# Kernel optimization log

Measured on AMD Instinct MI355X. Metric: run time of the kernel, lower is better.

The kernel has to match this reference:

```python
import jax, jax.numpy as jnp
import numpy as np

N_EMBD = 768
D_STATE = 64
D_CONV = 4
EXPAND = 2
D_INNER = N_EMBD * EXPAND  # 1536
DT_RANK = max(D_STATE // 16, 1)  # 4
BATCH, SEQ = 16, 512


def setup_inputs() -> dict:
    key = jax.random.key(0)
    ks = jax.random.split(key, 10)
    s = lambda fan_in: 1.0 / np.sqrt(fan_in)
    x = jax.random.normal(ks[0], (BATCH, SEQ, N_EMBD), dtype=jnp.float32)
    W_in = jax.random.uniform(ks[1], (N_EMBD, 2 * D_INNER), minval=-s(N_EMBD), maxval=s(N_EMBD))
    conv_w = jax.random.uniform(ks[2], (D_INNER, D_CONV), minval=-s(D_CONV), maxval=s(D_CONV))
    conv_b = jax.random.uniform(ks[3], (D_INNER,), minval=-s(D_CONV), maxval=s(D_CONV))
    W_x = jax.random.uniform(ks[4], (D_INNER, DT_RANK + 2 * D_STATE), minval=-s(D_INNER), maxval=s(D_INNER))
    W_dt = jax.random.uniform(ks[5], (DT_RANK, D_INNER), minval=-s(DT_RANK), maxval=s(DT_RANK))
    b_dt = jax.random.uniform(ks[6], (D_INNER,), minval=-s(DT_RANK), maxval=s(DT_RANK))
    # A_log = log(arange(1, N+1)) repeated per channel (S4D-real init)
    A_log = jnp.tile(jnp.log(jnp.arange(1, D_STATE + 1, dtype=jnp.float32))[None, :], (D_INNER, 1))
    Dp = jnp.ones((D_INNER,), dtype=jnp.float32)
    W_out = jax.random.uniform(ks[7], (D_INNER, N_EMBD), minval=-s(D_INNER), maxval=s(D_INNER))
    return {"x": x, "W_in": W_in, "conv_w": conv_w, "conv_b": conv_b,
            "W_x": W_x, "W_dt": W_dt, "b_dt": b_dt, "A_log": A_log,
            "Dp": Dp, "W_out": W_out}


def _mamba_forward(x, W_in, conv_w, conv_b, W_x, W_dt, b_dt, A_log, Dp, W_out):
    Bsz, L, _ = x.shape
    d_inner = Dp.shape[0]
    n = A_log.shape[1]
    dt_rank = W_dt.shape[0]

    xr = x @ W_in                                  # (B, L, 2*d_inner)
    x_ssm, res = jnp.split(xr, 2, axis=-1)

    # causal depthwise conv1d
    xc = x_ssm.transpose(0, 2, 1)                  # (B, d_inner, L)
    kern = conv_w[:, None, :]                      # (d_inner, 1, K) grouped
    xc = jax.lax.conv_general_dilated(
        xc, kern, window_strides=(1,),
        padding=[(conv_w.shape[-1] - 1, 0)],
        feature_group_count=d_inner)
    xc = xc + conv_b[None, :, None]
    x_ssm = jax.nn.silu(xc.transpose(0, 2, 1))      # (B, L, d_inner)

    x_dbl = x_ssm @ W_x                            # (B, L, dt_rank + 2n)
    dlt = x_dbl[..., :dt_rank]
    Bv = x_dbl[..., dt_rank:dt_rank + n]           # (B, L, n)
    Cv = x_dbl[..., dt_rank + n:]                  # (B, L, n)
    delta = jax.nn.softplus(dlt @ W_dt + b_dt)     # (B, L, d_inner)

    A = -jnp.exp(A_log)                            # (d_inner, n)

    def step(h, inp):
        d_t, B_t, C_t, x_t = inp                   # (B,d_inner),(B,n),(B,n),(B,d_inner)
        dA = jnp.exp(d_t[:, :, None] * A)          # (B, d_inner, n)
        u = d_t[:, :, None] * B_t[:, None, :] * x_t[:, :, None]
        h = dA * h + u
        y_t = jnp.einsum('bn,bdn->bd', C_t, h)
        return h, y_t

    h0 = jnp.zeros((Bsz, d_inner, n), dtype=x.dtype)
    _, ys = jax.lax.scan(
        step, h0,
        (delta.transpose(1, 0, 2), Bv.transpose(1, 0, 2),
         Cv.transpose(1, 0, 2), x_ssm.transpose(1, 0, 2)))
    y = ys.transpose(1, 0, 2) + Dp * x_ssm         # (B, L, d_inner)

    out = (y * jax.nn.silu(res)) @ W_out           # (B, L, n_embd)
    return out


def reference(x, W_in, conv_w, conv_b, W_x, W_dt, b_dt, A_log, Dp, W_out):
    return _mamba_forward(x, W_in, conv_w, conv_b, W_x, W_dt, b_dt, A_log, Dp, W_out)
```

## Files before the change

### kernel.cpp

```cpp
#include <hip/hip_runtime.h>

using u16 = unsigned short;
typedef __bf16 bf16x8 __attribute__((ext_vector_type(8)));
typedef float f32x4 __attribute__((ext_vector_type(4)));
typedef float f32x2 __attribute__((ext_vector_type(2)));

__device__ __forceinline__ float bf2f(u16 u) {
  unsigned v = ((unsigned)u) << 16;
  float f;
  __builtin_memcpy(&f, &v, 4);
  return f;
}
__device__ __forceinline__ u16 f2bf(float f) {
  unsigned v;
  __builtin_memcpy(&v, &f, 4);
  v = v + 0x7FFFu + ((v >> 16) & 1u);
  return (u16)(v >> 16);
}

#define GLL16(gp, lp)                                            \
  __builtin_amdgcn_global_load_lds(                              \
      (const __attribute__((address_space(1))) void*)(gp),       \
      (__attribute__((address_space(3))) void*)(lp), 16, 0, 0)

#define DPP_ADD(v, ctrl)                                                      \
  ((v) + __int_as_float(__builtin_amdgcn_update_dpp(                          \
             0, __float_as_int(v), (ctrl), 0xf, 0xf, true)))

__device__ __forceinline__ f32x2 pk_fma(f32x2 a, f32x2 b, f32x2 c) {
  return __builtin_elementwise_fma(a, b, c);
}
#define VLO(v) __builtin_shufflevector((v), (v), 0, 1)
#define VHI(v) __builtin_shufflevector((v), (v), 2, 3)

__global__ __launch_bounds__(256) void split_bf16_kernel(
    const float* __restrict__ X, u16* __restrict__ H, u16* __restrict__ L) {
  const int i4 = (blockIdx.x * 256 + threadIdx.x) << 2;
  const float4 v = *(const float4*)(X + i4);
  ushort4 h, l;
  h.x = f2bf(v.x); l.x = f2bf(v.x - bf2f(h.x));
  h.y = f2bf(v.y); l.y = f2bf(v.y - bf2f(h.y));
  h.z = f2bf(v.z); l.z = f2bf(v.z - bf2f(h.z));
  h.w = f2bf(v.w); l.w = f2bf(v.w - bf2f(h.w));
  *(ushort4*)(H + i4) = h;
  *(ushort4*)(L + i4) = l;
}

__global__ __launch_bounds__(256) void split_gate_kernel(
    const float* __restrict__ Y, const float* __restrict__ sres,
    u16* __restrict__ H, u16* __restrict__ L) {
  const int i4 = (blockIdx.x * 256 + threadIdx.x) << 2;
  const float4 y = *(const float4*)(Y + i4);
  const float4 g = *(const float4*)(sres + i4);
  float4 v = make_float4(y.x * g.x, y.y * g.y, y.z * g.z, y.w * g.w);
  ushort4 h, l;
  h.x = f2bf(v.x); l.x = f2bf(v.x - bf2f(h.x));
  h.y = f2bf(v.y); l.y = f2bf(v.y - bf2f(h.y));
  h.z = f2bf(v.z); l.z = f2bf(v.z - bf2f(h.z));
  h.w = f2bf(v.w); l.w = f2bf(v.w - bf2f(h.w));
  *(ushort4*)(H + i4) = h;
  *(ushort4*)(L + i4) = l;
}

__global__ __launch_bounds__(256) void transpose_split_kernel(
    const float* __restrict__ W, int K, int N, u16* __restrict__ Thi,
    u16* __restrict__ Tlo) {
  __shared__ float t[32][33];
  const int tid = threadIdx.x;
  const int r = tid >> 3, c4 = (tid & 7) << 2;
  const float4 v = *(const float4*)(W + (size_t)(blockIdx.y * 32 + r) * N +
                                    blockIdx.x * 32 + c4);
  t[r][c4 + 0] = v.x;
  t[r][c4 + 1] = v.y;
  t[r][c4 + 2] = v.z;
  t[r][c4 + 3] = v.w;
  __syncthreads();
  const float w0 = t[c4 + 0][r], w1 = t[c4 + 1][r];
  const float w2 = t[c4 + 2][r], w3 = t[c4 + 3][r];
  ushort4 h, l;
  h.x = f2bf(w0); l.x = f2bf(w0 - bf2f(h.x));
  h.y = f2bf(w1); l.y = f2bf(w1 - bf2f(h.y));
  h.z = f2bf(w2); l.z = f2bf(w2 - bf2f(h.z));
  h.w = f2bf(w3); l.w = f2bf(w3 - bf2f(h.w));
  const size_t o = (size_t)(blockIdx.x * 32 + r) * K + blockIdx.y * 32 + c4;
  *(ushort4*)(Thi + o) = h;
  *(ushort4*)(Tlo + o) = l;
}

template <int BM, int BN, int WM, int WN, int NTILES, int EPI>
__global__ __launch_bounds__(64 * WM * WN, 2) void gemm_pipe(
    const u16* __restrict__ Ahi, const u16* __restrict__ Alo,
    const u16* __restrict__ BThi, const u16* __restrict__ BTlo,
    float* __restrict__ C0, float* __restrict__ C1, int N, int nSplit) {
  constexpr int T = 64 * WM * WN;
  constexpr int K = NTILES * 32;
  constexpr int RW = BM / WM;
  constexpr int CW = BN / WN;
  constexpr int MT = RW / 16;
  constexpr int NC = CW / 16;
  constexpr int IA = BM / (T / 4);
  constexpr int IB = BN / (T / 4);
  constexpr int L = 2 * (IA + IB);
  constexpr int OAl = BM * 32;
  constexpr int OBh = 2 * BM * 32;
  constexpr int OBl = 2 * BM * 32 + BN * 32;
  constexpr int SBUF = 2 * (BM + BN) * 32;

  extern __shared__ u16 S[];

  const int tid = threadIdx.x;
  const int lane = tid & 63, wv = tid >> 6;
  const int wm = wv / WN, wn = wv % WN;
  const int bm0 = blockIdx.y * BM, bn0 = blockIdx.x * BN;
  const int fr = lane & 15, fq = lane >> 4;
  const int rq = tid >> 2;
  const int cq = (tid & 3) << 3;

  f32x4 acc[MT][NC];
#pragma unroll
  for (int i = 0; i < MT; ++i)
#pragma unroll
    for (int j = 0; j < NC; ++j) acc[i][j] = {0.f, 0.f, 0.f, 0.f};

  auto stage = [&](int kt, int sbuf) {
    const int k0 = kt * 32;
    u16* Sb = S + sbuf * SBUF;
#pragma unroll
    for (int i = 0; i < IA; ++i) {
      const size_t g = (size_t)(bm0 + i * (T / 4) + rq) * K + k0 + cq;
      const int lb = (i * (T / 4) + wv * 16) * 32;
      GLL16(Ahi + g, Sb + lb);
      GLL16(Alo + g, Sb + OAl + lb);
    }
#pragma unroll
    for (int i = 0; i < IB; ++i) {
      const size_t g = (size_t)(bn0 + i * (T / 4) + rq) * K + k0 + cq;
      const int lb = (i * (T / 4) + wv * 16) * 32;
      GLL16(BThi + g, Sb + OBh + lb);
      GLL16(BTlo + g, Sb + OBl + lb);
    }
  };

  stage(0, 0);
  stage(1, 1);
  asm volatile("s_waitcnt vmcnt(%0)" ::"i"(L) : "memory");
  __builtin_amdgcn_s_barrier();
  __builtin_amdgcn_sched_barrier(0);

  int cb = 0, sb = 2;
#pragma unroll 3
  for (int t = 0; t < NTILES; ++t) {
    if (t + 2 < NTILES) stage(t + 2, sb);

    const u16* Sb = S + cb * SBUF;
    bf16x8 fAh[MT], fAl[MT], fBh[NC], fBl[NC];
#pragma unroll
    for (int mt = 0; mt < MT; ++mt) {
      const int ao = (wm * RW + mt * 16 + fr) * 32 + fq * 8;
      fAh[mt] = *(const bf16x8*)&Sb[ao];
      fAl[mt] = *(const bf16x8*)&Sb[OAl + ao];
    }
#pragma unroll
    for (int nt = 0; nt < NC; ++nt) {
      const int bo = (wn * CW + nt * 16 + fr) * 32 + fq * 8;
      fBh[nt] = *(const bf16x8*)&Sb[OBh + bo];
      fBl[nt] = *(const bf16x8*)&Sb[OBl + bo];
    }

    __builtin_amdgcn_s_setprio(1);
#pragma unroll
    for (int mt = 0; mt < MT; ++mt)
#pragma unroll
      for (int nt = 0; nt < NC; ++nt) {
        acc[mt][nt] = __builtin_amdgcn_mfma_f32_16x16x32_bf16(
            fAh[mt], fBh[nt], acc[mt][nt], 0, 0, 0);
        acc[mt][nt] = __builtin_amdgcn_mfma_f32_16x16x32_bf16(
            fAh[mt], fBl[nt], acc[mt][nt], 0, 0, 0);
        acc[mt][nt] = __builtin_amdgcn_mfma_f32_16x16x32_bf16(
            fAl[mt], fBh[nt], acc[mt][nt], 0, 0, 0);
      }
    __builtin_amdgcn_s_setprio(0);

    if (t + 1 < NTILES) {
      if (t + 2 < NTILES) {
        asm volatile("s_waitcnt vmcnt(%0)" ::"i"(L) : "memory");
      } else {
        asm volatile("s_waitcnt vmcnt(0)" ::: "memory");
      }
      __builtin_amdgcn_s_barrier();
      __builtin_amdgcn_sched_barrier(0);
    }
    cb = cb == 2 ? 0 : cb + 1;
    sb = sb == 2 ? 0 : sb + 1;
  }

#pragma unroll
  for (int mt = 0; mt < MT; ++mt)
#pragma unroll
    for (int nt = 0; nt < NC; ++nt) {
      const int col = bn0 + wn * CW + nt * 16 + fr;
#pragma unroll
      for (int r = 0; r < 4; ++r) {
        const int row = bm0 + wm * RW + mt * 16 + fq * 4 + r;
        float v = acc[mt][nt][r];
        if (EPI == 1) {
          if (col < nSplit) {
            C0[(size_t)row * nSplit + col] = v;
          } else {
            v = v / (1.f + __expf(-v));
            C1[(size_t)row * (N - nSplit) + (col - nSplit)] = v;
          }
        } else {
          C0[(size_t)row * N + col] = v;
        }
      }
    }
}

__global__ __launch_bounds__(256) void conv_silu_kernel(
    const float* __restrict__ raw, const float* __restrict__ cw,
    const float* __restrict__ cb, float* __restrict__ xs) {
  const int i4 = (blockIdx.x * 256 + threadIdx.x) << 2;
  const int d = i4 % 1536;
  const int l = (i4 / 1536) & 511;
  const float4 wA = *(const float4*)(cw + (d << 2));
  const float4 wB = *(const float4*)(cw + (d << 2) + 4);
  const float4 wC = *(const float4*)(cw + (d << 2) + 8);
  const float4 wD = *(const float4*)(cw + (d << 2) + 12);
  float4 acc = *(const float4*)(cb + d);
  const float* p = raw + i4;
  const float4 x3 = *(const float4*)(p);
  acc.x = fmaf(x3.x, wA.w, acc.x);
  acc.y = fmaf(x3.y, wB.w, acc.y);
  acc.z = fmaf(x3.z, wC.w, acc.z);
  acc.w = fmaf(x3.w, wD.w, acc.w);
  if (l >= 3) {
    const float4 x0 = *(const float4*)(p - 4608);
    const float4 x1 = *(const float4*)(p - 3072);
    const float4 x2 = *(const float4*)(p - 1536);
    acc.x = fmaf(x0.x, wA.x, acc.x); acc.y = fmaf(x0.y, wB.x, acc.y);
    acc.z = fmaf(x0.z, wC.x, acc.z); acc.w = fmaf(x0.w, wD.x, acc.w);
    acc.x = fmaf(x1.x, wA.y, acc.x); acc.y = fmaf(x1.y, wB.y, acc.y);
    acc.z = fmaf(x1.z, wC.y, acc.z); acc.w = fmaf(x1.w, wD.y, acc.w);
    acc.x = fmaf(x2.x, wA.z, acc.x); acc.y = fmaf(x2.y, wB.z, acc.y);
    acc.z = fmaf(x2.z, wC.z, acc.z); acc.w = fmaf(x2.w, wD.z, acc.w);
  } else {
#pragma unroll
    for (int k = 0; k < 3; ++k) {
      if (l - 3 + k >= 0) {
        const float4 xk = *(const float4*)(p + (k - 3) * 1536);
        const float wkA = (&wA.x)[k], wkB = (&wB.x)[k];
        const float wkC = (&wC.x)[k], wkD = (&wD.x)[k];
        acc.x = fmaf(xk.x, wkA, acc.x);
        acc.y = fmaf(xk.y, wkB, acc.y);
        acc.z = fmaf(xk.z, wkC, acc.z);
        acc.w = fmaf(xk.w, wkD, acc.w);
      }
    }
  }
  float4 o;
  o.x = acc.x / (1.f + __expf(-acc.x));
  o.y = acc.y / (1.f + __expf(-acc.y));
  o.z = acc.z / (1.f + __expf(-acc.z));
  o.w = acc.w / (1.f + __expf(-acc.w));
  *(float4*)(xs + i4) = o;
}

__global__ __launch_bounds__(256) void gemm_x_kernel(
    const float* __restrict__ XS, const float* __restrict__ Wx,
    float* __restrict__ Xd) {
  __shared__ float rows[8 * 1536];
  const int tid = threadIdx.x;
  const float4* src = (const float4*)(XS + (size_t)blockIdx.x * (8 * 1536));
  float4* dst = (float4*)rows;
#pragma unroll
  for (int j = 0; j < 12; ++j) dst[tid + 256 * j] = src[tid + 256 * j];
  __syncthreads();
  if (tid < 132) {
    float acc[8];
#pragma unroll
    for (int r = 0; r < 8; ++r) acc[r] = 0.f;
    for (int k = 0; k < 1536; k += 4) {
      const float w0 = Wx[(k + 0) * 132 + tid];
      const float w1 = Wx[(k + 1) * 132 + tid];
      const float w2 = Wx[(k + 2) * 132 + tid];
      const float w3 = Wx[(k + 3) * 132 + tid];
#pragma unroll
      for (int r = 0; r < 8; ++r) {
        const float4 xr = *(const float4*)&rows[r * 1536 + k];
        acc[r] = fmaf(xr.x, w0, acc[r]);
        acc[r] = fmaf(xr.y, w1, acc[r]);
        acc[r] = fmaf(xr.z, w2, acc[r]);
        acc[r] = fmaf(xr.w, w3, acc[r]);
      }
    }
    float* out = Xd + (size_t)blockIdx.x * (8 * 132) + tid;
#pragma unroll
    for (int r = 0; r < 8; ++r) out[r * 132] = acc[r];
  }
}

__global__ __launch_bounds__(256) void delta_kernel(
    const float* __restrict__ Xd, const float* __restrict__ Wdt,
    const float* __restrict__ bdt, float* __restrict__ delta) {
  const int i4 = (blockIdx.x * 256 + threadIdx.x) << 2;
  const int d = i4 % 1536;
  const int bl = i4 / 1536;
  const float4 t = *(const float4*)(Xd + (size_t)bl * 132);
  const float4 W0 = *(const float4*)(Wdt + d);
  const float4 W1 = *(const float4*)(Wdt + 1536 + d);
  const float4 W2 = *(const float4*)(Wdt + 3072 + d);
  const float4 W3 = *(const float4*)(Wdt + 4608 + d);
  float4 z = *(const float4*)(bdt + d);
  z.x = fmaf(t.x, W0.x, z.x); z.y = fmaf(t.x, W0.y, z.y);
  z.z = fmaf(t.x, W0.z, z.z); z.w = fmaf(t.x, W0.w, z.w);
  z.x = fmaf(t.y, W1.x, z.x); z.y = fmaf(t.y, W1.y, z.y);
  z.z = fmaf(t.y, W1.z, z.z); z.w = fmaf(t.y, W1.w, z.w);
  z.x = fmaf(t.z, W2.x, z.x); z.y = fmaf(t.z, W2.y, z.y);
  z.z = fmaf(t.z, W2.z, z.z); z.w = fmaf(t.z, W2.w, z.w);
  z.x = fmaf(t.w, W3.x, z.x); z.y = fmaf(t.w, W3.y, z.y);
  z.z = fmaf(t.w, W3.z, z.z); z.w = fmaf(t.w, W3.w, z.w);
  float4 o;
  o.x = fmaxf(z.x, 0.f) + log1pf(__expf(-fabsf(z.x)));
  o.y = fmaxf(z.y, 0.f) + log1pf(__expf(-fabsf(z.y)));
  o.z = fmaxf(z.z, 0.f) + log1pf(__expf(-fabsf(z.z)));
  o.w = fmaxf(z.w, 0.f) + log1pf(__expf(-fabsf(z.w)));
  *(float4*)(delta + i4) = o;
}

__global__ __launch_bounds__(256) void scan_kernel(
    const float* __restrict__ delta, float* __restrict__ xs,
    const float* __restrict__ Xd, const float* __restrict__ Dp) {
  __shared__ float L[2][16 * 192];
  const int tid = threadIdx.x;
  const int lane = tid & 63;
  const int wv = tid >> 6;
  const int ln = (lane & 3) | ((lane >> 1) & 4);
  const int sub = ((lane >> 2) & 1) | ((lane >> 3) & 6);
  const int b = blockIdx.x / 48;
  const int dg = blockIdx.x - b * 48;
  const int dbase = dg << 5;
  const int ch = (wv << 3) + sub;
  const int d = dbase + ch;

  const float dp = Dp[d];
  const float cln = -(float)(8 * ln);

  const size_t blBase = (size_t)b * 512;
  float* pYl = xs + (blBase + (size_t)ln) * 1536 + d;

  int sj[4], sf[4];
#pragma unroll
  for (int s = 0; s < 4; ++s) {
    const int u = tid + (s << 8);
    sj[s] = u >> 6;
    sf[s] = u & 63;
  }

  const int idxD = 128 + ch;
  const int idxX = 160 + ch;
  const int ofsB = ln << 3;
  const int ofsC = 64 + (ln << 3);

  float4 st[4];
#define STAGE_LOAD(c)                                                         \
  {                                                                           \
    _Pragma("unroll") for (int s = 0; s < 4; ++s) {                           \
      const int f = sf[s];                                                    \
      if (f < 48) {                                                           \
        const size_t bl = blBase + ((c) << 4) + sj[s];                        \
        const float* src =                                                    \
            (f < 32) ? (Xd + bl * 132 + 4 + (f << 2))                         \
                     : ((f < 40) ? (delta + bl * 1536 + dbase + ((f - 32) << 2)) \
                                 : (xs + bl * 1536 + dbase + ((f - 40) << 2))); \
        st[s] = *(const float4*)src;                                          \
      }                                                                       \
    }                                                                         \
  }
#define STAGE_WRITE(c)                                                        \
  {                                                                           \
    float* Lb = &L[(c) & 1][0];                                               \
    _Pragma("unroll") for (int s = 0; s < 4; ++s) {                           \
      const int f = sf[s];                                                    \
      if (f < 48) {                                                           \
        const int di = sj[s] * 192 +                                          \
                       ((f < 32) ? (f << 2)                                   \
                                 : ((f < 40) ? (128 + ((f - 32) << 2))        \
                                             : (160 + ((f - 40) << 2))));     \
        *(float4*)&Lb[di] = st[s];                                            \
      }                                                                       \
    }                                                                         \
  }

  f32x2 H0 = {0.f, 0.f}, H1 = {0.f, 0.f}, H2 = {0.f, 0.f}, H3 = {0.f, 0.f};
  float yacc = 0.f;

  STAGE_LOAD(0);
  STAGE_WRITE(0);
  __syncthreads();

  for (int c = 0; c < 32; ++c) {
    if (c < 31) STAGE_LOAD(c + 1);
    const float* P = &L[c & 1][0];
#pragma unroll
    for (int j = 0; j < 16; ++j) {
      const float dl = P[j * 192 + idxD];
      const float xt = P[j * 192 + idxX];
      const f32x4 Bq0 = *(const f32x4*)&P[j * 192 + ofsB];
      const f32x4 Bq1 = *(const f32x4*)&P[j * 192 + ofsB + 4];
      const f32x4 Cq0 = *(const f32x4*)&P[j * 192 + ofsC];
      const f32x4 Cq1 = *(const f32x4*)&P[j * 192 + ofsC + 4];

      const float r = __expf(-dl);
      const float e0 = __expf(cln * dl);
      const float dx = dl * xt;
      const float r2 = r * r;
      f32x2 Q0;
      Q0[0] = e0 * r;
      Q0[1] = Q0[0] * r;
      const f32x2 r2v = {r2, r2};
      const f32x2 Q1 = Q0 * r2v;
      const f32x2 Q2 = Q1 * r2v;
      const f32x2 Q3 = Q2 * r2v;
      const f32x2 dxv = {dx, dx};

      H0 = pk_fma(Q0, H0, dxv * VLO(Bq0));
      H1 = pk_fma(Q1, H1, dxv * VHI(Bq0));
      H2 = pk_fma(Q2, H2, dxv * VLO(Bq1));
      H3 = pk_fma(Q3, H3, dxv * VHI(Bq1));

      f32x2 Pv = VLO(Cq0) * H0;
      Pv = pk_fma(VHI(Cq0), H1, Pv);
      Pv = pk_fma(VLO(Cq1), H2, Pv);
      Pv = pk_fma(VHI(Cq1), H3, Pv);
      float p = Pv[0] + Pv[1];
      p = DPP_ADD(p, 0xB1);
      p = DPP_ADD(p, 0x4E);
      p = DPP_ADD(p, 0x128);
      const float yv = fmaf(dp, xt, p);
      yacc = (ln == (j & 7)) ? yv : yacc;
      if ((j & 7) == 7) {
        pYl[(size_t)((c << 4) + (j & 8)) * 1536] = yacc;
      }
    }
    if (c < 31) STAGE_WRITE(c + 1);
    __syncthreads();
  }
#undef STAGE_LOAD
#undef STAGE_WRITE
}

extern "C" void kernel_launch(void* const* d_in, const int* in_sizes, int n_in,
                              void* d_out, int out_size, void* d_ws,
                              size_t ws_size, hipStream_t stream) {
  const float* x = (const float*)d_in[0];
  const float* W_in = (const float*)d_in[1];
  const float* conv_w = (const float*)d_in[2];
  const float* conv_b = (const float*)d_in[3];
  const float* W_x = (const float*)d_in[4];
  const float* W_dt = (const float*)d_in[5];
  const float* b_dt = (const float*)d_in[6];
  const float* Dp = (const float*)d_in[8];
  const float* W_out = (const float*)d_in[9];

  char* ws = (char*)d_ws;
  float* raw = (float*)(ws);
  char* Dreg = ws + 50331648;
  u16* xhi = (u16*)(Dreg);
  u16* xlo = (u16*)(Dreg + 12582912);
  u16* WinThi = (u16*)(Dreg + 25165824);
  u16* WinTlo = (u16*)(Dreg + 29884416);
  float* xs = (float*)(Dreg);
  float* res = (float*)(ws + 100663296);
  float* xdbl = (float*)(ws + 150994944);
  float* delta = raw;
  u16* yhi = (u16*)(ws);
  u16* ylo = (u16*)(ws + 25165824);
  u16* WoutThi = (u16*)(ws + 100663296);
  u16* WoutTlo = (u16*)(ws + 100663296 + 2359296);

  static bool attr_done = false;
  if (!attr_done) {
    hipFuncSetAttribute(
        reinterpret_cast<const void*>(&gemm_pipe<256, 128, 4, 2, 24, 1>),
        hipFuncAttributeMaxDynamicSharedMemorySize, 147456);
    hipFuncSetAttribute(
        reinterpret_cast<const void*>(&gemm_pipe<256, 128, 4, 2, 48, 0>),
        hipFuncAttributeMaxDynamicSharedMemorySize, 147456);
    attr_done = true;
  }

  dim3 blk(256);
  hipLaunchKernelGGL(split_bf16_kernel, dim3(6144), blk, 0, stream, x, xhi,
                     xlo);
  hipLaunchKernelGGL(transpose_split_kernel, dim3(96, 24), blk, 0, stream,
                     W_in, 768, 3072, WinThi, WinTlo);
  hipLaunchKernelGGL((gemm_pipe<256, 128, 4, 2, 24, 1>), dim3(24, 32),
                     dim3(512), 147456, stream, xhi, xlo, WinThi, WinTlo, raw,
                     res, 3072, 1536);
  hipLaunchKernelGGL(conv_silu_kernel, dim3(12288), blk, 0, stream, raw,
                     conv_w, conv_b, xs);
  hipLaunchKernelGGL(gemm_x_kernel, dim3(1024), blk, 0, stream, xs, W_x, xdbl);
  hipLaunchKernelGGL(delta_kernel, dim3(12288), blk, 0, stream, xdbl, W_dt,
                     b_dt, delta);
  hipLaunchKernelGGL(scan_kernel, dim3(768), blk, 0, stream, delta, xs, xdbl,
                     Dp);
  hipLaunchKernelGGL(split_gate_kernel, dim3(12288), blk, 0, stream, xs, res,
                     yhi, ylo);
  hipLaunchKernelGGL(transpose_split_kernel, dim3(24, 48), blk, 0, stream,
                     W_out, 1536, 768, WoutThi, WoutTlo);
  hipLaunchKernelGGL((gemm_pipe<256, 128, 4, 2, 48, 0>), dim3(6, 32),
                     dim3(512), 147456, stream, yhi, ylo, WoutThi, WoutTlo,
                     (float*)d_out, nullptr, 768, 0);
}
```

Baseline: 705.8 us.

## Move x_proj GEMM onto MFMA with split-bf16 three-pass emulation

Replaces the scalar fp32 x_ssm @ W_x kernel with an MFMA-based GEMM. It uses hi/lo bf16 splits of both operands and three products to keep close to fp32 accuracy. A new prep kernel transposes W_x into padded (144-row) hi/lo bf16 buffers in the workspace. The GEMM double-buffers LDS, converts A on the fly and stages B through global_load_lds. This adds an extra launch and a conversion step, and uses only 256 blocks of 128 threads.

```diff
diff --git a/kernel.cpp b/kernel.cpp
--- a/kernel.cpp
+++ b/kernel.cpp
@@ -87,6 +87,34 @@
   *(ushort4*)(Tlo + o) = l;
 }
 
+__global__ __launch_bounds__(256) void wxt_prep_kernel(
+    const float* __restrict__ Wx, u16* __restrict__ Thi,
+    u16* __restrict__ Tlo) {
+  __shared__ float t[32][33];
+  const int tid = threadIdx.x;
+  const int r = tid >> 3, c4 = (tid & 7) << 2;
+#pragma unroll
+  for (int j = 0; j < 4; ++j) {
+    const int n = blockIdx.x * 32 + c4 + j;
+    t[r][c4 + j] =
+        (n < 132) ? Wx[(size_t)(blockIdx.y * 32 + r) * 132 + n] : 0.f;
+  }
+  __syncthreads();
+  const int nrow = blockIdx.x * 32 + r;
+  if (nrow < 144) {
+    const float w0 = t[c4 + 0][r], w1 = t[c4 + 1][r];
+    const float w2 = t[c4 + 2][r], w3 = t[c4 + 3][r];
+    ushort4 h, l;
+    h.x = f2bf(w0); l.x = f2bf(w0 - bf2f(h.x));
+    h.y = f2bf(w1); l.y = f2bf(w1 - bf2f(h.y));
+    h.z = f2bf(w2); l.z = f2bf(w2 - bf2f(h.z));
+    h.w = f2bf(w3); l.w = f2bf(w3 - bf2f(h.w));
+    const size_t o = (size_t)nrow * 1536 + blockIdx.y * 32 + c4;
+    *(ushort4*)(Thi + o) = h;
+    *(ushort4*)(Tlo + o) = l;
+  }
+}
+
 template <int BM, int BN, int WM, int WN, int NTILES, int EPI>
 __global__ __launch_bounds__(64 * WM * WN, 2) void gemm_pipe(
     const u16* __restrict__ Ahi, const u16* __restrict__ Alo,
@@ -215,6 +243,111 @@
         }
       }
     }
+}
+
+__global__ __launch_bounds__(128) void gemm_xp_kernel(
+    const float* __restrict__ XS, const u16* __restrict__ BThi,
+    const u16* __restrict__ BTlo, float* __restrict__ Xd) {
+  __shared__ u16 sA[2][2][32 * 32];
+  __shared__ u16 sB[2][2][144 * 32];
+  const int tid = threadIdx.x;
+  const int lane = tid & 63, wv = tid >> 6;
+  const int bm0 = blockIdx.x << 5;
+  const int fr = lane & 15, fq = lane >> 4;
+  const int ar = tid >> 2, ac = (tid & 3) << 3;
+
+  f32x4 acc[9];
+#pragma unroll
+  for (int j = 0; j < 9; ++j) acc[j] = {0.f, 0.f, 0.f, 0.f};
+
+  const float* pA = XS + (size_t)(bm0 + ar) * 1536 + ac;
+
+  float4 xa0, xa1;
+  auto loadA = [&](int k0) {
+    xa0 = *(const float4*)(pA + k0);
+    xa1 = *(const float4*)(pA + k0 + 4);
+  };
+  auto writeA = [&](int buf) {
+    ushort4 h0, h1, l0, l1;
+    h0.x = f2bf(xa0.x); l0.x = f2bf(xa0.x - bf2f(h0.x));
+    h0.y = f2bf(xa0.y); l0.y = f2bf(xa0.y - bf2f(h0.y));
+    h0.z = f2bf(xa0.z); l0.z = f2bf(xa0.z - bf2f(h0.z));
+    h0.w = f2bf(xa0.w); l0.w = f2bf(xa0.w - bf2f(h0.w));
+    h1.x = f2bf(xa1.x); l1.x = f2bf(xa1.x - bf2f(h1.x));
+    h1.y = f2bf(xa1.y); l1.y = f2bf(xa1.y - bf2f(h1.y));
+    h1.z = f2bf(xa1.z); l1.z = f2bf(xa1.z - bf2f(h1.z));
+    h1.w = f2bf(xa1.w); l1.w = f2bf(xa1.w - bf2f(h1.w));
+    u16* Ah = &sA[buf][0][ar * 32 + ac];
+    u16* Al = &sA[buf][1][ar * 32 + ac];
+    *(ushort4*)Ah = h0;
+    *(ushort4*)(Ah + 4) = h1;
+    *(ushort4*)Al = l0;
+    *(ushort4*)(Al + 4) = l1;
+  };
+  auto stageB = [&](int k0, int buf) {
+#pragma unroll
+    for (int i = 0; i < 5; ++i) {
+      const int ch = i * 128 + tid;
+      if (ch < 576) {
+        const int row = ch >> 2, cq = (ch & 3) << 3;
+        const size_t g = (size_t)row * 1536 + k0 + cq;
+        u16* lb = &sB[buf][0][0] + (size_t)(i * 128 + wv * 64) * 8;
+        GLL16(BThi + g, lb);
+        GLL16(BTlo + g, lb + 144 * 32);
+      }
+    }
+  };
+
+  loadA(0);
+  stageB(0, 0);
+  writeA(0);
+  __syncthreads();
+
+  int buf = 0;
+  for (int t = 0; t < 48; ++t) {
+    if (t + 1 < 48) {
+      loadA((t + 1) * 32);
+      stageB((t + 1) * 32, buf ^ 1);
+    }
+    {
+      const u16* Ah = &sA[buf][0][0];
+      const u16* Al = &sA[buf][1][0];
+      const u16* Bh = &sB[buf][0][0];
+      const u16* Bl = &sB[buf][1][0];
+      const int ao = (wv * 16 + fr) * 32 + fq * 8;
+      const bf16x8 fAh = *(const bf16x8*)&Ah[ao];
+      const bf16x8 fAl = *(const bf16x8*)&Al[ao];
+      __builtin_amdgcn_s_setprio(1);
+#pragma unroll
+      for (int nt = 0; nt < 9; ++nt) {
+        const int bo = (nt * 16 + fr) * 32 + fq * 8;
+        const bf16x8 fBh = *(const bf16x8*)&Bh[bo];
+        const bf16x8 fBl = *(const bf16x8*)&Bl[bo];
+        acc[nt] = __builtin_amdgcn_mfma_f32_16x16x32_bf16(fAh, fBh, acc[nt],
+                                                          0, 0, 0);
+        acc[nt] = __builtin_amdgcn_mfma_f32_16x16x32_bf16(fAh, fBl, acc[nt],
+                                                          0, 0, 0);
+        acc[nt] = __builtin_amdgcn_mfma_f32_16x16x32_bf16(fAl, fBh, acc[nt],
+                                                          0, 0, 0);
+      }
+      __builtin_amdgcn_s_setprio(0);
+    }
+    if (t + 1 < 48) writeA(buf ^ 1);
+    __syncthreads();
+    buf ^= 1;
+  }
+
+#pragma unroll
+  for (int nt = 0; nt < 9; ++nt) {
+    const int col = nt * 16 + fr;
+    if (col < 132) {
+#pragma unroll
+      for (int r = 0; r < 4; ++r) {
+        const int row = bm0 + wv * 16 + fq * 4 + r;
+        Xd[(size_t)row * 132 + col] = acc[nt][r];
+      }
+    }
+  }
 }
 
 __global__ __launch_bounds__(256) void conv_silu_kernel(
@@ -266,40 +399,6 @@
   *(float4*)(xs + i4) = o;
 }
 
-__global__ __launch_bounds__(256) void gemm_x_kernel(
-    const float* __restrict__ XS, const float* __restrict__ Wx,
-    float* __restrict__ Xd) {
-  __shared__ float rows[8 * 1536];
-  const int tid = threadIdx.x;
-  const float4* src = (const float4*)(XS + (size_t)blockIdx.x * (8 * 1536));
-  float4* dst = (float4*)rows;
-#pragma unroll
-  for (int j = 0; j < 12; ++j) dst[tid + 256 * j] = src[tid + 256 * j];
-  __syncthreads();
-  if (tid < 132) {
-    float acc[8];
-#pragma unroll
-    for (int r = 0; r < 8; ++r) acc[r] = 0.f;
-    for (int k = 0; k < 1536; k += 4) {
-      const float w0 = Wx[(k + 0) * 132 + tid];
-      const float w1 = Wx[(k + 1) * 132 + tid];
-      const float w2 = Wx[(k + 2) * 132 + tid];
-      const float w3 = Wx[(k + 3) * 132 + tid];
-#pragma unroll
-      for (int r = 0; r < 8; ++r) {
-        const float4 xr = *(const float4*)&rows[r * 1536 + k];
-        acc[r] = fmaf(xr.x, w0, acc[r]);
-        acc[r] = fmaf(xr.y, w1, acc[r]);
-        acc[r] = fmaf(xr.z, w2, acc[r]);
-        acc[r] = fmaf(xr.w, w3, acc[r]);
-      }
-    }
-    float* out = Xd + (size_t)blockIdx.x * (8 * 132) + tid;
-#pragma unroll
-    for (int r = 0; r < 8; ++r) out[r * 132] = acc[r];
-  }
-}
-
 __global__ __launch_bounds__(256) void delta_kernel(
     const float* __restrict__ Xd, const float* __restrict__ Wdt,
     const float* __restrict__ bdt, float* __restrict__ delta) {
@@ -474,6 +573,8 @@
   float* res = (float*)(ws + 100663296);
   float* xdbl = (float*)(ws + 150994944);
   float* delta = raw;
+  u16* WxThi = (u16*)(ws);
+  u16* WxTlo = (u16*)(ws + 442368);
   u16* yhi = (u16*)(ws);
   u16* ylo = (u16*)(ws + 25165824);
   u16* WoutThi = (u16*)(ws + 100663296);
@@ -500,7 +601,10 @@
                      res, 3072, 1536);
   hipLaunchKernelGGL(conv_silu_kernel, dim3(12288), blk, 0, stream, raw,
                      conv_w, conv_b, xs);
-  hipLaunchKernelGGL(gemm_x_kernel, dim3(1024), blk, 0, stream, xs, W_x, xdbl);
+  hipLaunchKernelGGL(wxt_prep_kernel, dim3(5, 48), blk, 0, stream, W_x,
+                     WxThi, WxTlo);
+  hipLaunchKernelGGL(gemm_xp_kernel, dim3(256), dim3(128), 0, stream, xs,
+                     WxThi, WxTlo, xdbl);
   hipLaunchKernelGGL(delta_kernel, dim3(12288), blk, 0, stream, xdbl, W_dt,
                      b_dt, delta);
   hipLaunchKernelGGL(scan_kernel, dim3(768), blk, 0, stream, delta, xs, xdbl,
```

Result: faster. 604.2 us (-14.4%).
